# Optimization experiments

Hardware: AMD Instinct MI355X
Metric: run time of the kernel (lower is better)

Reference implementation:

```python
import jax, jax.numpy as jnp
import numpy as np

B, T, NQ, H = 32, 64, 128, 128


def setup_inputs() -> dict:
    key = jax.random.key(0)
    ks = jax.random.split(key, 16)
    n = lambda k, s, sc=0.05: jax.random.normal(k, s, dtype=jnp.float32) * sc
    return {
        "q": jax.random.randint(ks[0], (B, T), 0, NQ),
        "r": jax.random.randint(ks[1], (B, T), 0, 2),
        "x_emb_table": n(ks[2], (2 * NQ, H)),
        "q_emb": n(ks[3], (NQ, H)),
        "init_h": n(ks[4], (NQ, H)),
        "w1": n(ks[5], (H, 2 * H)),
        "b1": n(ks[6], (H,)),
        "w2": n(ks[7], (H, H)),
        "b2": n(ks[8], (H,)),
        "w_ih": n(ks[9], (3 * H, 2 * H)),
        "w_hh": n(ks[10], (3 * H, H)),
        "b_ih": n(ks[11], (3 * H,)),
        "b_hh": n(ks[12], (3 * H,)),
        "bias": n(ks[13], (1, NQ, 1)),
        "out_w": n(ks[14], (1, H)),
    }


def _gru_over_nodes(u, w_ih, w_hh, b_ih, b_hh):
    # Faithful to torch nn.GRU(batch_first=True) applied to [B, NQ, 2H]:
    # it recurs over the num_q axis with h0 = 0.
    h_dim = w_hh.shape[1]
    gi = jnp.einsum('bni,gi->bng', u, w_ih) + b_ih  # [B, NQ, 3H], input part precomputed

    def step(h, gi_t):  # h: [B, H], gi_t: [B, 3H]
        gh = h @ w_hh.T + b_hh
        ir, iz, inn = jnp.split(gi_t, 3, axis=-1)
        hr, hz, hn = jnp.split(gh, 3, axis=-1)
        rg = jax.nn.sigmoid(ir + hr)
        zg = jax.nn.sigmoid(iz + hz)
        ng = jnp.tanh(inn + rg * hn)
        h_new = (1.0 - zg) * ng + zg * h
        return h_new, h_new

    h0 = jnp.zeros((u.shape[0], h_dim), u.dtype)
    _, hs = jax.lax.scan(step, h0, jnp.swapaxes(gi, 0, 1))  # over NQ
    return jnp.swapaxes(hs, 0, 1)  # [B, NQ, H]


def reference(q, r, x_emb_table, q_emb, init_h, w1, b1, w2, b2,
              w_ih, w_hh, b_ih, b_hh, bias, out_w):
    bsz = q.shape[0]
    nq, hdim = q_emb.shape
    x = q + nq * r                                  # [B, T]
    x_emb = x_emb_table[x]                          # [B, T, H]
    qoh = jax.nn.one_hot(q, nq, dtype=x_emb.dtype)  # [B, T, NQ]
    ht0 = jnp.broadcast_to(init_h[None], (bsz, nq, hdim))

    def step(ht, inputs):
        xt, mask = inputs                # xt: [B,H], mask: [B,NQ]
        m3 = mask[..., None]             # [B, NQ, 1]
        # aggregate: second half is xt where qt matches, else q_emb; first half is ht either way
        other = m3 * xt[:, None, :] + (1.0 - m3) * q_emb[None]
        ht_ = jnp.concatenate([ht, other], axis=-1)          # [B, NQ, 2H]
        # update: f_neighbor is unimplemented (None->0); m = onehot * f_self(ht_)
        hs_mlp = jax.nn.relu(ht_ @ w1.T + b1) @ w2.T + b2    # mlp (eval: dropout=id)
        m = m3 * hs_mlp
        u = jnp.concatenate([m, ht], axis=-1)                # [B, NQ, 2H]
        ht_new = _gru_over_nodes(u, w_ih, w_hh, b_ih, b_hh)  # [B, NQ, H]
        yt = jax.nn.sigmoid(jnp.squeeze(ht_new @ out_w.T + bias, -1))  # [B, NQ]
        return ht_new, (ht_new, yt)

    _, (hs, ys) = jax.lax.scan(
        step, ht0, (jnp.swapaxes(x_emb, 0, 1), jnp.swapaxes(qoh, 0, 1)))
    h = jnp.concatenate([ht0[:, None], jnp.swapaxes(hs, 0, 1)], axis=1)  # [B, T+1, NQ, H]
    y = jnp.swapaxes(ys, 0, 1)                                           # [B, T, NQ]
    return y, h
```

## Files before the change

### kernel.cpp

```cpp
#include <hip/hip_runtime.h>

#define BB 32
#define TT 64
#define NQl 128
#define HD 128
#define CPAD 524
#define HPAD 132

typedef _Float16 f16x8 __attribute__((ext_vector_type(8)));
typedef float f32x16 __attribute__((ext_vector_type(16)));
typedef float f32x4 __attribute__((ext_vector_type(4)));

__device__ __forceinline__ float sigmoidf_(float x) {
  return __builtin_amdgcn_rcpf(1.f + __expf(-x));
}
__device__ __forceinline__ float tanhf_(float x) {
  float a = fminf(fabsf(x), 15.f);
  float e = __expf(-2.f * a);
  float t = (1.f - e) * __builtin_amdgcn_rcpf(1.f + e);
  return copysignf(t, x);
}
__device__ __forceinline__ float dot4_(f32x4 a, f32x4 b) {
  return a[0] * b[0] + a[1] * b[1] + a[2] * b[2] + a[3] * b[3];
}
__device__ __forceinline__ f16x8 pack_frag_h(f32x4 a, f32x4 b) {
  f16x8 o;
  o[0] = (_Float16)a[0]; o[1] = (_Float16)a[1];
  o[2] = (_Float16)a[2]; o[3] = (_Float16)a[3];
  o[4] = (_Float16)b[0]; o[5] = (_Float16)b[1];
  o[6] = (_Float16)b[2]; o[7] = (_Float16)b[3];
  return o;
}
__device__ __forceinline__ uint4 pack8_h(const float v[8]) {
  union { f16x8 h; uint4 u; } c;
#pragma unroll
  for (int i = 0; i < 8; ++i) c.h[i] = (_Float16)v[i];
  return c.u;
}

__device__ __forceinline__ void issue_load32_cc(const float* p, f32x4& a, f32x4& b) {
  asm volatile(
      "global_load_dwordx4 %0, %2, off sc1\n\t"
      "global_load_dwordx4 %1, %2, off offset:16 sc1"
      : "=&v"(a), "=&v"(b) : "v"(p) : "memory");
}
__device__ __forceinline__ void wait_vm0_2(f32x4& a, f32x4& b) {
  asm volatile("s_waitcnt vmcnt(0)" : "+v"(a), "+v"(b) :: "memory");
  __builtin_amdgcn_sched_barrier(0);
}
__device__ __forceinline__ void store32_cc(float* p, f32x4 a, f32x4 b) {
  asm volatile(
      "global_store_dwordx4 %0, %1, off sc1\n\t"
      "global_store_dwordx4 %0, %2, off offset:16 sc1"
      :: "v"(p), "v"(a), "v"(b) : "memory");
}

#define CHAIN(NS, S0, FR, BIASV, OUTCOL)                                        \
  {                                                                             \
    f32x16 acc;                                                                 \
    _Pragma("unroll")                                                           \
    for (int i = 0; i < 16; ++i) acc[i] = (BIASV);                              \
    _Pragma("unroll")                                                           \
    for (int ks = 0; ks < (NS); ++ks) {                                         \
      unsigned int off = ((unsigned int)(((S0) + ks) * 32 + (lhi << 4))) ^ swz; \
      f16x8 av = *(const f16x8*)(smA + rowbase + off);                          \
      acc = __builtin_amdgcn_mfma_f32_32x32x16_f16(av, FR[ks], acc, 0, 0, 0);   \
    }                                                                           \
    _Pragma("unroll")                                                           \
    for (int rg = 0; rg < 16; ++rg) {                                           \
      int br = (rg & 3) + 8 * (rg >> 2) + 4 * lhi;                              \
      sC[br * CPAD + (OUTCOL)] = acc[rg];                                       \
    }                                                                           \
  }

__global__ void __launch_bounds__(512, 2) gkt_wavefront(
    const int* __restrict__ qp, const int* __restrict__ rp_,
    const float* __restrict__ x_emb, const float* __restrict__ init_h,
    const float* __restrict__ w1, const float* __restrict__ b1,
    const float* __restrict__ w2, const float* __restrict__ b2,
    const float* __restrict__ w_ih, const float* __restrict__ w_hh,
    const float* __restrict__ b_ih, const float* __restrict__ b_hh,
    const float* __restrict__ bias, const float* __restrict__ out_w,
    float* __restrict__ y_out, float* h_out, int* flags, int* ticket) {
  __shared__ __align__(16) unsigned char smA[32 * 512];
  __shared__ float sC[32 * CPAD];
  __shared__ float sHrun[32 * HPAD];
  __shared__ float sHtp[32 * HPAD];
  __shared__ float sXt[32 * HPAD];
  __shared__ float sRed[4 * HPAD];
  __shared__ float sV1[128], sV2[128];
  __shared__ float sBias[128], sOutW[128], sB1[128], sB2[128];
  __shared__ unsigned int sMask[128];
  __shared__ int sTicket;

  const int tid = threadIdx.x;
  const int lane = tid & 63;
  const int wv = tid >> 6;
  const int l31 = lane & 31;
  const int lhi = lane >> 5;

  if (tid == 0) sTicket = atomicAdd(ticket, 1);
  __syncthreads();
  const int t = sTicket;

  if (tid < 128) {
    sBias[tid] = bias[tid];
    sOutW[tid] = out_w[tid];
    sB1[tid] = b1[tid];
    sB2[tid] = b2[tid];
    sMask[tid] = 0u;
  }
  for (int i = tid; i < 32 * HPAD; i += 512) sHrun[i] = 0.f;
  __syncthreads();
  if (tid < 32) {
    int qb = qp[tid * TT + t];
    atomicOr(&sMask[qb], 1u << tid);
  }

  const int b = tid >> 4;
  const int f = tid & 15;
  const unsigned int swzb = (unsigned int)((b & 7) << 4);
  {
    int qb = qp[b * TT + t];
    int rb = rp_[b * TT + t];
    const float* src = x_emb + (size_t)(qb + NQl * rb) * HD + f * 8;
    *(f32x4*)(sXt + b * HPAD + f * 8) = *(const f32x4*)src;
    *(f32x4*)(sXt + b * HPAD + f * 8 + 4) = *(const f32x4*)(src + 4);
    *(uint4*)(smA + b * 512 + ((unsigned int)(256 + f * 16) ^ swzb)) = make_uint4(0, 0, 0, 0);
  }

  const int gcol = wv * 32 + l31;
  f16x8 Brz[16];
#pragma unroll
  for (int ks = 0; ks < 16; ++ks) {
    const float* src = (ks < 8)
        ? (w_ih + (size_t)gcol * 256 + 128 + ks * 16 + lhi * 8)
        : (w_hh + (size_t)gcol * 128 + (ks - 8) * 16 + lhi * 8);
    Brz[ks] = pack_frag_h(*(const f32x4*)src, *(const f32x4*)(src + 4));
  }
  const int ecol = (wv < 4) ? (256 + wv * 32 + l31) : (384 + (wv - 4) * 32 + l31);
  const int erow = (wv < 4) ? ecol : (ecol - 128);
  f16x8 Bex[8];
#pragma unroll
  for (int ks = 0; ks < 8; ++ks) {
    const float* src = (wv < 4)
        ? (w_ih + (size_t)erow * 256 + 128 + ks * 16 + lhi * 8)
        : (w_hh + (size_t)erow * 128 + ks * 16 + lhi * 8);
    Bex[ks] = pack_frag_h(*(const f32x4*)src, *(const f32x4*)(src + 4));
  }
  const float brz = b_ih[gcol] + b_hh[gcol];
  const float bex = (wv < 4) ? b_ih[ecol] : b_hh[erow];

  float* hstore_base = h_out + (((size_t)b * (TT + 1) + (t + 1)) * NQl) * HD + f * 8;
  const float* hload_base = h_out + (((size_t)b * (TT + 1) + t) * NQl) * HD + f * 8;

  if (t == 0) {
    const f32x4* s4 = (const f32x4*)init_h;
    for (int i = tid; i < 32 * 4096; i += 512) {
      int bb = i >> 12, rem = i & 4095;
      ((f32x4*)(h_out + ((size_t)bb * (TT + 1)) * NQl * HD))[rem] = s4[rem];
    }
  }

  {
    float v[8];
    if (t > 0) {
      if (lane == 0) {
        int c = 0;
        while (__hip_atomic_load(&flags[(t - 1) * NQl + 0], __ATOMIC_RELAXED,
                                 __HIP_MEMORY_SCOPE_AGENT) == 0) {
          __builtin_amdgcn_s_sleep(1);
          if (++c > (1 << 20)) break;
        }
      }
      f32x4 a0, a1;
      issue_load32_cc(hload_base, a0, a1);
      wait_vm0_2(a0, a1);
      *(f32x4*)&v[0] = a0; *(f32x4*)&v[4] = a1;
    } else {
      const float* src = init_h + f * 8;
      *(f32x4*)&v[0] = *(const f32x4*)src;
      *(f32x4*)&v[4] = *(const f32x4*)(src + 4);
    }
    *(f32x4*)(sHtp + b * HPAD + f * 8) = *(f32x4*)&v[0];
    *(f32x4*)(sHtp + b * HPAD + f * 8 + 4) = *(f32x4*)&v[4];
    *(uint4*)(smA + b * 512 + ((unsigned int)(f * 16) ^ swzb)) = pack8_h(v);
  }
  __syncthreads();

  const int rowbase = l31 * 512;
  const unsigned int swz = (unsigned int)((l31 & 7) << 4);

  for (int n = 0; n < NQl; ++n) {
    CHAIN(16, 0, Brz, brz, gcol)
    if (wv < 4) { CHAIN(8, 0, Bex, bex, ecol) } else { CHAIN(8, 8, Bex, bex, ecol) }
    __syncthreads();

    unsigned int mk = sMask[n];
    while (mk) {
      const int b0 = __ffs(mk) - 1;
      mk &= mk - 1;
      {
        const int j = tid & 127, kq = tid >> 7;
        const float* wr = w1 + (size_t)j * 256 + kq * 64;
        const float* xr = (kq < 2) ? (sHtp + b0 * HPAD + kq * 64)
                                   : (sXt + b0 * HPAD + (kq - 2) * 64);
        float s = 0.f;
#pragma unroll
        for (int ii = 0; ii < 16; ++ii)
          s += dot4_(*(const f32x4*)(wr + ii * 4), *(const f32x4*)(xr + ii * 4));
        sRed[kq * HPAD + j] = s;
      }
      __syncthreads();
      if (tid < 128) {
        float v = sB1[tid] + sRed[tid] + sRed[HPAD + tid] + sRed[2 * HPAD + tid] +
                  sRed[3 * HPAD + tid];
        sV1[tid] = fmaxf(v, 0.f);
      }
      __syncthreads();
      {
        const int j = tid & 127, kq = tid >> 7;
        const float* wr = w2 + (size_t)j * 128 + kq * 32;
        const float* xr = sV1 + kq * 32;
        float s = 0.f;
#pragma unroll
        for (int ii = 0; ii < 8; ++ii)
          s += dot4_(*(const f32x4*)(wr + ii * 4), *(const f32x4*)(xr + ii * 4));
        sRed[kq * HPAD + j] = s;
      }
      __syncthreads();
      if (tid < 128)
        sV2[tid] = sB2[tid] + sRed[tid] + sRed[HPAD + tid] + sRed[2 * HPAD + tid] +
                   sRed[3 * HPAD + tid];
      __syncthreads();
      if (tid < 384) {
        const float* wr = w_ih + (size_t)tid * 256;
        float s = 0.f;
#pragma unroll
        for (int ii = 0; ii < 32; ++ii)
          s += dot4_(*(const f32x4*)(wr + ii * 4), *(const f32x4*)(sV2 + ii * 4));
        sC[b0 * CPAD + tid] += s;
      }
      __syncthreads();
    }

    const int nn = n + 1;
    f32x4 p0, p1;
    if (nn < NQl) {
      if (t > 0) {
        if (lane == 0) {
          int c = 0;
          while (__hip_atomic_load(&flags[(t - 1) * NQl + nn], __ATOMIC_RELAXED,
                                   __HIP_MEMORY_SCOPE_AGENT) == 0) {
            __builtin_amdgcn_s_sleep(1);
            if (++c > (1 << 20)) break;
          }
        }
        issue_load32_cc(hload_base + (size_t)nn * HD, p0, p1);
      } else {
        const float* src = init_h + (size_t)nn * HD + f * 8;
        p0 = *(const f32x4*)src;
        p1 = *(const f32x4*)(src + 4);
      }
    }

    {
      const int j0 = f * 8;
      const float* Cb = sC + b * CPAD;
      float rpre[8], zpre[8], ipre[8], hpre[8], hold[8];
      *(f32x4*)&rpre[0] = *(const f32x4*)(Cb + j0);
      *(f32x4*)&rpre[4] = *(const f32x4*)(Cb + j0 + 4);
      *(f32x4*)&zpre[0] = *(const f32x4*)(Cb + 128 + j0);
      *(f32x4*)&zpre[4] = *(const f32x4*)(Cb + 128 + j0 + 4);
      *(f32x4*)&ipre[0] = *(const f32x4*)(Cb + 256 + j0);
      *(f32x4*)&ipre[4] = *(const f32x4*)(Cb + 256 + j0 + 4);
      *(f32x4*)&hpre[0] = *(const f32x4*)(Cb + 384 + j0);
      *(f32x4*)&hpre[4] = *(const f32x4*)(Cb + 384 + j0 + 4);
      *(f32x4*)&hold[0] = *(const f32x4*)(sHrun + b * HPAD + j0);
      *(f32x4*)&hold[4] = *(const f32x4*)(sHrun + b * HPAD + j0 + 4);
      float hnew[8];
      float yp = 0.f;
#pragma unroll
      for (int i = 0; i < 8; ++i) {
        float rg = sigmoidf_(rpre[i]);
        float zg = sigmoidf_(zpre[i]);
        float ng = tanhf_(ipre[i] + rg * hpre[i]);
        float hv = ng + zg * (hold[i] - ng);
        hnew[i] = hv;
        yp += hv * sOutW[j0 + i];
      }
      *(f32x4*)(sHrun + b * HPAD + j0) = *(f32x4*)&hnew[0];
      *(f32x4*)(sHrun + b * HPAD + j0 + 4) = *(f32x4*)&hnew[4];
      *(uint4*)(smA + b * 512 + ((unsigned int)(256 + f * 16) ^ swzb)) = pack8_h(hnew);
      store32_cc(hstore_base + (size_t)n * HD, *(f32x4*)&hnew[0], *(f32x4*)&hnew[4]);
      yp += __shfl_xor(yp, 1);
      yp += __shfl_xor(yp, 2);
      yp += __shfl_xor(yp, 4);
      yp += __shfl_xor(yp, 8);
      if (f == 0) {
        float yv = sigmoidf_(yp + sBias[n]);
        y_out[((size_t)b * TT + t) * NQl + n] = yv;
      }
    }

    if (nn < NQl) {
      if (t > 0) wait_vm0_2(p0, p1);
      float v[8];
      *(f32x4*)&v[0] = p0; *(f32x4*)&v[4] = p1;
      *(f32x4*)(sHtp + b * HPAD + f * 8) = p0;
      *(f32x4*)(sHtp + b * HPAD + f * 8 + 4) = p1;
      *(uint4*)(smA + b * 512 + ((unsigned int)(f * 16) ^ swzb)) = pack8_h(v);
    }
    asm volatile("s_waitcnt vmcnt(0)" ::: "memory");
    __syncthreads();
    if (tid == 0)
      __hip_atomic_store(&flags[t * NQl + n], 1, __ATOMIC_RELAXED,
                         __HIP_MEMORY_SCOPE_AGENT);
  }
}

extern "C" void kernel_launch(void* const* d_in, const int* in_sizes, int n_in,
                              void* d_out, int out_size, void* d_ws, size_t ws_size,
                              hipStream_t stream) {
  (void)in_sizes; (void)n_in; (void)out_size; (void)ws_size;
  const int* q = (const int*)d_in[0];
  const int* r = (const int*)d_in[1];
  const float* x_emb = (const float*)d_in[2];
  const float* init_h = (const float*)d_in[4];
  const float* w1 = (const float*)d_in[5];
  const float* b1 = (const float*)d_in[6];
  const float* w2 = (const float*)d_in[7];
  const float* b2 = (const float*)d_in[8];
  const float* w_ih = (const float*)d_in[9];
  const float* w_hh = (const float*)d_in[10];
  const float* b_ih = (const float*)d_in[11];
  const float* b_hh = (const float*)d_in[12];
  const float* bias = (const float*)d_in[13];
  const float* out_w = (const float*)d_in[14];

  float* y_out = (float*)d_out;
  float* h_out = y_out + (size_t)BB * TT * NQl;
  int* flags = (int*)d_ws;
  int* ticket = flags + TT * NQl;

  hipMemsetAsync(d_ws, 0, (TT * NQl + 16) * sizeof(int), stream);
  gkt_wavefront<<<TT, 512, 0, stream>>>(q, r, x_emb, init_h, w1, b1, w2, b2,
                                        w_ih, w_hh, b_ih, b_hh, bias, out_w,
                                        y_out, h_out, flags, ticket);
}
```

Baseline: 2.653 ms.

## Replace block barrier flag publish with per-wave counters and overlap next-row prefetch

Each wave now increments the per-(t,n) flag itself once its own stores drain, and consumers wait until the count reaches 8. This removes the trailing block-wide barrier before the flag is published. sHtp is double-buffered so the next row's prefetched h can be written while the MLP branch still reads the current row. The MLP branch is moved after the prefetch issue, the y reduction is moved after the publish, and the init_h copy for t=0 is spread across all blocks. In exchange it relies on per-wave ordering of memory operations and on atomic read-modify-write polling, which adds traffic on the flags.

Result: slower. 3.050 ms (+15.0%).

```diff
diff --git a/kernel.cpp b/kernel.cpp
--- a/kernel.cpp
+++ b/kernel.cpp
@@ -53,6 +53,13 @@
       "global_store_dwordx4 %0, %1, off sc1\n\t"
       "global_store_dwordx4 %0, %2, off offset:16 sc1"
       :: "v"(p), "v"(a), "v"(b) : "memory");
+}
+
+__device__ __forceinline__ int flag_read_rmw(int* p) {
+  return __hip_atomic_fetch_add(p, 0, __ATOMIC_RELAXED, __HIP_MEMORY_SCOPE_AGENT);
+}
+__device__ __forceinline__ void flag_add1(int* p) {
+  __hip_atomic_fetch_add(p, 1, __ATOMIC_RELAXED, __HIP_MEMORY_SCOPE_AGENT);
 }
 
 #define CHAIN(NS, S0, FR, BIASV, OUTCOL)                                        \
@@ -85,8 +92,8 @@
   __shared__ __align__(16) unsigned char smA[32 * 512];
   __shared__ float sC[32 * CPAD];
   __shared__ float sHrun[32 * HPAD];
-  __shared__ float sHtp[32 * HPAD];
-  __shared__ float sXt[32 * HPAD];
+  __shared__ float sHtp[2][32 * HPAD];
+  __shared__ float sXt[32 * 128];
   __shared__ float sRed[4 * HPAD];
   __shared__ float sV1[128], sV2[128];
   __shared__ float sBias[128], sOutW[128], sB1[128], sB2[128];
@@ -124,8 +131,8 @@
     int qb = qp[b * TT + t];
     int rb = rp_[b * TT + t];
     const float* src = x_emb + (size_t)(qb + NQl * rb) * HD + f * 8;
-    *(f32x4*)(sXt + b * HPAD + f * 8) = *(const f32x4*)src;
-    *(f32x4*)(sXt + b * HPAD + f * 8 + 4) = *(const f32x4*)(src + 4);
+    *(f32x4*)(sXt + b * 128 + f * 8) = *(const f32x4*)src;
+    *(f32x4*)(sXt + b * 128 + f * 8 + 4) = *(const f32x4*)(src + 4);
     *(uint4*)(smA + b * 512 + ((unsigned int)(256 + f * 16) ^ swzb)) = make_uint4(0, 0, 0, 0);
   }
 
@@ -154,9 +161,9 @@
   float* hstore_base = h_out + (((size_t)b * (TT + 1) + (t + 1)) * NQl) * HD + f * 8;
   const float* hload_base = h_out + (((size_t)b * (TT + 1) + t) * NQl) * HD + f * 8;
 
-  if (t == 0) {
+  {
     const f32x4* s4 = (const f32x4*)init_h;
-    for (int i = tid; i < 32 * 4096; i += 512) {
+    for (int i = t * 512 + tid; i < 32 * 4096; i += TT * 512) {
       int bb = i >> 12, rem = i & 4095;
       ((f32x4*)(h_out + ((size_t)bb * (TT + 1)) * NQl * HD))[rem] = s4[rem];
     }
@@ -167,9 +174,8 @@
     if (t > 0) {
       if (lane == 0) {
         int c = 0;
-        while (__hip_atomic_load(&flags[(t - 1) * NQl + 0], __ATOMIC_RELAXED,
-                                 __HIP_MEMORY_SCOPE_AGENT) == 0) {
-          __builtin_amdgcn_s_sleep(1);
+        while (flag_read_rmw(&flags[(t - 1) * NQl + 0]) < 8) {
+          __builtin_amdgcn_s_sleep(2);
           if (++c > (1 << 20)) break;
         }
       }
@@ -182,67 +188,20 @@
       *(f32x4*)&v[0] = *(const f32x4*)src;
       *(f32x4*)&v[4] = *(const f32x4*)(src + 4);
     }
-    *(f32x4*)(sHtp + b * HPAD + f * 8) = *(f32x4*)&v[0];
-    *(f32x4*)(sHtp + b * HPAD + f * 8 + 4) = *(f32x4*)&v[4];
+    *(f32x4*)(sHtp[0] + b * HPAD + f * 8) = *(f32x4*)&v[0];
+    *(f32x4*)(sHtp[0] + b * HPAD + f * 8 + 4) = *(f32x4*)&v[4];
     *(uint4*)(smA + b * 512 + ((unsigned int)(f * 16) ^ swzb)) = pack8_h(v);
   }
-  __syncthreads();
 
   const int rowbase = l31 * 512;
   const unsigned int swz = (unsigned int)((l31 & 7) << 4);
 
   for (int n = 0; n < NQl; ++n) {
+    __syncthreads();
+
     CHAIN(16, 0, Brz, brz, gcol)
     if (wv < 4) { CHAIN(8, 0, Bex, bex, ecol) } else { CHAIN(8, 8, Bex, bex, ecol) }
     __syncthreads();
-
-    unsigned int mk = sMask[n];
-    while (mk) {
-      const int b0 = __ffs(mk) - 1;
-      mk &= mk - 1;
-      {
-        const int j = tid & 127, kq = tid >> 7;
-        const float* wr = w1 + (size_t)j * 256 + kq * 64;
-        const float* xr = (kq < 2) ? (sHtp + b0 * HPAD + kq * 64)
-                                   : (sXt + b0 * HPAD + (kq - 2) * 64);
-        float s = 0.f;
-#pragma unroll
-        for (int ii = 0; ii < 16; ++ii)
-          s += dot4_(*(const f32x4*)(wr + ii * 4), *(const f32x4*)(xr + ii * 4));
-        sRed[kq * HPAD + j] = s;
-      }
-      __syncthreads();
-      if (tid < 128) {
-        float v = sB1[tid] + sRed[tid] + sRed[HPAD + tid] + sRed[2 * HPAD + tid] +
-                  sRed[3 * HPAD + tid];
-        sV1[tid] = fmaxf(v, 0.f);
-      }
-      __syncthreads();
-      {
-        const int j = tid & 127, kq = tid >> 7;
-        const float* wr = w2 + (size_t)j * 128 + kq * 32;
-        const float* xr = sV1 + kq * 32;
-        float s = 0.f;
-#pragma unroll
-        for (int ii = 0; ii < 8; ++ii)
-          s += dot4_(*(const f32x4*)(wr + ii * 4), *(const f32x4*)(xr + ii * 4));
-        sRed[kq * HPAD + j] = s;
-      }
-      __syncthreads();
-      if (tid < 128)
-        sV2[tid] = sB2[tid] + sRed[tid] + sRed[HPAD + tid] + sRed[2 * HPAD + tid] +
-                   sRed[3 * HPAD + tid];
-      __syncthreads();
-      if (tid < 384) {
-        const float* wr = w_ih + (size_t)tid * 256;
-        float s = 0.f;
-#pragma unroll
-        for (int ii = 0; ii < 32; ++ii)
-          s += dot4_(*(const f32x4*)(wr + ii * 4), *(const f32x4*)(sV2 + ii * 4));
-        sC[b0 * CPAD + tid] += s;
-      }
-      __syncthreads();
-    }
 
     const int nn = n + 1;
     f32x4 p0, p1;
@@ -250,9 +209,8 @@
       if (t > 0) {
         if (lane == 0) {
           int c = 0;
-          while (__hip_atomic_load(&flags[(t - 1) * NQl + nn], __ATOMIC_RELAXED,
-                                   __HIP_MEMORY_SCOPE_AGENT) == 0) {
-            __builtin_amdgcn_s_sleep(1);
+          while (flag_read_rmw(&flags[(t - 1) * NQl + nn]) < 8) {
+            __builtin_amdgcn_s_sleep(2);
             if (++c > (1 << 20)) break;
           }
         }
@@ -264,6 +222,56 @@
       }
     }
 
+    unsigned int mk = sMask[n];
+    while (mk) {
+      const int b0 = __ffs(mk) - 1;
+      mk &= mk - 1;
+      const float* htp_row = sHtp[n & 1] + b0 * HPAD;
+      {
+        const int j = tid & 127, kq = tid >> 7;
+        const float* wr = w1 + (size_t)j * 256 + kq * 64;
+        const float* xr = (kq < 2) ? (htp_row + kq * 64)
+                                   : (sXt + b0 * 128 + (kq - 2) * 64);
+        float s = 0.f;
+#pragma unroll
+        for (int ii = 0; ii < 16; ++ii)
+          s += dot4_(*(const f32x4*)(wr + ii * 4), *(const f32x4*)(xr + ii * 4));
+        sRed[kq * HPAD + j] = s;
+      }
+      __syncthreads();
+      if (tid < 128) {
+        float v = sB1[tid] + sRed[tid] + sRed[HPAD + tid] + sRed[2 * HPAD + tid] +
+                  sRed[3 * HPAD + tid];
+        sV1[tid] = fmaxf(v, 0.f);
+      }
+      __syncthreads();
+      {
+        const int j = tid & 127, kq = tid >> 7;
+        const float* wr = w2 + (size_t)j * 128 + kq * 32;
+        const float* xr = sV1 + kq * 32;
+        float s = 0.f;
+#pragma unroll
+        for (int ii = 0; ii < 8; ++ii)
+          s += dot4_(*(const f32x4*)(wr + ii * 4), *(const f32x4*)(xr + ii * 4));
+        sRed[kq * HPAD + j] = s;
+      }
+      __syncthreads();
+      if (tid < 128)
+        sV2[tid] = sB2[tid] + sRed[tid] + sRed[HPAD + tid] + sRed[2 * HPAD + tid] +
+                   sRed[3 * HPAD + tid];
+      __syncthreads();
+      if (tid < 384) {
+        const float* wr = w_ih + (size_t)tid * 256;
+        float s = 0.f;
+#pragma unroll
+        for (int ii = 0; ii < 32; ++ii)
+          s += dot4_(*(const f32x4*)(wr + ii * 4), *(const f32x4*)(sV2 + ii * 4));
+        sC[b0 * CPAD + tid] += s;
+      }
+      __syncthreads();
+    }
+
+    float yp = 0.f;
     {
       const int j0 = f * 8;
       const float* Cb = sC + b * CPAD;
@@ -279,7 +287,6 @@
       *(f32x4*)&hold[0] = *(const f32x4*)(sHrun + b * HPAD + j0);
       *(f32x4*)&hold[4] = *(const f32x4*)(sHrun + b * HPAD + j0 + 4);
       float hnew[8];
-      float yp = 0.f;
 #pragma unroll
       for (int i = 0; i < 8; ++i) {
         float rg = sigmoidf_(rpre[i]);
@@ -293,29 +300,30 @@
       *(f32x4*)(sHrun + b * HPAD + j0 + 4) = *(f32x4*)&hnew[4];
       *(uint4*)(smA + b * 512 + ((unsigned int)(256 + f * 16) ^ swzb)) = pack8_h(hnew);
       store32_cc(hstore_base + (size_t)n * HD, *(f32x4*)&hnew[0], *(f32x4*)&hnew[4]);
-      yp += __shfl_xor(yp, 1);
-      yp += __shfl_xor(yp, 2);
-      yp += __shfl_xor(yp, 4);
-      yp += __shfl_xor(yp, 8);
-      if (f == 0) {
-        float yv = sigmoidf_(yp + sBias[n]);
-        y_out[((size_t)b * TT + t) * NQl + n] = yv;
-      }
-    }
+    }
+
+    if (nn < NQl && t > 0) {
+      wait_vm0_2(p0, p1);
+    } else {
+      asm volatile("s_waitcnt vmcnt(0)" ::: "memory");
+    }
+    if (lane == 0) flag_add1(&flags[t * NQl + n]);
 
     if (nn < NQl) {
-      if (t > 0) wait_vm0_2(p0, p1);
       float v[8];
       *(f32x4*)&v[0] = p0; *(f32x4*)&v[4] = p1;
-      *(f32x4*)(sHtp + b * HPAD + f * 8) = p0;
-      *(f32x4*)(sHtp + b * HPAD + f * 8 + 4) = p1;
+      *(f32x4*)(sHtp[nn & 1] + b * HPAD + f * 8) = p0;
+      *(f32x4*)(sHtp[nn & 1] + b * HPAD + f * 8 + 4) = p1;
       *(uint4*)(smA + b * 512 + ((unsigned int)(f * 16) ^ swzb)) = pack8_h(v);
     }
-    asm volatile("s_waitcnt vmcnt(0)" ::: "memory");
-    __syncthreads();
-    if (tid == 0)
-      __hip_atomic_store(&flags[t * NQl + n], 1, __ATOMIC_RELAXED,
-                         __HIP_MEMORY_SCOPE_AGENT);
+    yp += __shfl_xor(yp, 1);
+    yp += __shfl_xor(yp, 2);
+    yp += __shfl_xor(yp, 4);
+    yp += __shfl_xor(yp, 8);
+    if (f == 0) {
+      float yv = sigmoidf_(yp + sBias[n]);
+      y_out[((size_t)b * TT + t) * NQl + n] = yv;
+    }
   }
 }
 
```
